# Kernel tuning notes

Hardware: AMD Instinct MI355X
Metric: run time of the kernel (lower is better)

The kernel has to match this reference:

```python
import jax, jax.numpy as jnp
import numpy as np

FIRE_RATE = 0.5
ANGLE = 0.0

def _sobel_kernels(angle=ANGLE):
    dx = np.outer([1, 2, 1], [-1, 0, 1]) / 8.0
    dy = dx.T
    c = np.cos(angle * np.pi / 180.0)
    s = np.sin(angle * np.pi / 180.0)
    w1 = (c * dx - s * dy).astype(np.float32)
    w2 = (s * dx + c * dy).astype(np.float32)
    # torch applies conv after transpose(1,3) so its spatial axes are (W,H);
    # transposing kernels makes our NHWC conv over (H,W) match exactly.
    return jnp.asarray(w1.T), jnp.asarray(w2.T)

def _depthwise3x3(x, w):
    # x: [B,H,W,C], w: [3,3] shared across all C channels (groups=C)
    C = x.shape[-1]
    k = jnp.tile(w[:, :, None, None], (1, 1, 1, C))  # [3,3,1,C] HWIO
    return jax.lax.conv_general_dilated(
        x, k, window_strides=(1, 1), padding='SAME',
        dimension_numbers=('NHWC', 'HWIO', 'NHWC'),
        feature_group_count=C)

def setup_inputs() -> dict:
    key = jax.random.key(0)
    k1, k2, k3 = jax.random.split(key, 3)
    B, H, W, C, HID = 8, 256, 256, 16, 128
    x = jax.random.uniform(k1, (B, H, W, C), dtype=jnp.float32)
    # xavier-uniform-like init for fc0/fc1
    lim0 = float(np.sqrt(6.0 / (3 * C + HID)))
    lim1 = float(np.sqrt(6.0 / (HID + C)))
    W0 = jax.random.uniform(k2, (HID, 3 * C), minval=-lim0, maxval=lim0, dtype=jnp.float32)
    b0 = jnp.zeros((HID,), dtype=jnp.float32)
    W1 = jax.random.uniform(k3, (C, HID), minval=-lim1, maxval=lim1, dtype=jnp.float32)
    return {'x': x, 'W0': W0, 'b0': b0, 'W1': W1, 'steps': 2}

def reference(x, W0, b0, W1, steps):
    w1, w2 = _sobel_kernels()
    key = jax.random.key(42)
    for step in range(steps):
        # perceive: identity + two depthwise sobel filters -> [B,H,W,3C]
        y = jnp.concatenate([x, _depthwise3x3(x, w1), _depthwise3x3(x, w2)], axis=-1)
        # per-cell MLP
        h = jax.nn.relu(jnp.einsum('bhwk,ok->bhwo', y, W0) + b0)
        dx = jnp.einsum('bhwo,co->bhwc', h, W1)
        # stochastic fire-rate mask [B,H,W,1]
        mk = jax.random.fold_in(key, step)
        mask = (jax.random.uniform(mk, dx.shape[:3] + (1,)) > FIRE_RATE).astype(dx.dtype)
        new = x + dx * mask
        # only channels 3: are updated (first 3 channels stay fixed)
        x = jnp.concatenate([x[..., :3], new[..., 3:]], axis=-1)
    return x
```

## Files before the change

### kernel.cpp

```cpp
#include <hip/hip_runtime.h>
#include <hip/hip_bf16.h>
#include <stdint.h>


#define NB 8
#define NH 256
#define NW 256
#define NC 16
#define WOFF 65536

typedef __attribute__((ext_vector_type(8))) short short8;
typedef __attribute__((ext_vector_type(4))) float floatx4;

__host__ __device__ inline void tf2x32(uint32_t k0, uint32_t k1,
                                       uint32_t x0, uint32_t x1,
                                       uint32_t& o0, uint32_t& o1) {
  const uint32_t ks2 = k0 ^ k1 ^ 0x1BD11BDAu;
  x0 += k0; x1 += k1;
#define RL(v, d) (((v) << (d)) | ((v) >> (32 - (d))))
#define R4(a, b, c, d)                          \
  x0 += x1; x1 = RL(x1, a); x1 ^= x0;           \
  x0 += x1; x1 = RL(x1, b); x1 ^= x0;           \
  x0 += x1; x1 = RL(x1, c); x1 ^= x0;           \
  x0 += x1; x1 = RL(x1, d); x1 ^= x0;
  R4(13, 15, 26, 6);  x0 += k1;  x1 += ks2 + 1u;
  R4(17, 29, 16, 24); x0 += ks2; x1 += k0 + 2u;
  R4(13, 15, 26, 6);  x0 += k0;  x1 += k1 + 3u;
  R4(17, 29, 16, 24); x0 += k1;  x1 += ks2 + 4u;
  R4(13, 15, 26, 6);  x0 += ks2; x1 += k0 + 5u;
#undef R4
#undef RL
  o0 = x0; o1 = x1;
}

__device__ inline short bfr(float x) {
  __hip_bfloat16 h = __float2bfloat16(x);
  return *reinterpret_cast<short*>(&h);
}

__global__ __launch_bounds__(64) void ca_prep(
    const float* __restrict__ W0, const float* __restrict__ b0,
    const float* __restrict__ W1, short* __restrict__ wbuf) {
  const int lane = threadIdx.x;
  const int c15 = lane & 15;
  const int g = lane >> 4;
  const int fi = blockIdx.x;
  short8 f;
  if (fi < 16) {
    const int n = fi >> 1;
    const int o = 16 * n + c15;
    if ((fi & 1) == 0) {
      const float s0 = (g < 2) ? 1.0f : 0.125f;
      const float* p = W0 + o * 48 + 8 * g;
      const floatx4 v0 = *reinterpret_cast<const floatx4*>(p);
      const floatx4 v1 = *reinterpret_cast<const floatx4*>(p + 4);
      f[0] = bfr(v0.x * s0); f[1] = bfr(v0.y * s0);
      f[2] = bfr(v0.z * s0); f[3] = bfr(v0.w * s0);
      f[4] = bfr(v1.x * s0); f[5] = bfr(v1.y * s0);
      f[6] = bfr(v1.z * s0); f[7] = bfr(v1.w * s0);
    } else {
      if (g < 2) {
        const float* p1 = W0 + o * 48 + 32 + 8 * g;
        const floatx4 u0 = *reinterpret_cast<const floatx4*>(p1);
        const floatx4 u1 = *reinterpret_cast<const floatx4*>(p1 + 4);
        f[0] = bfr(u0.x * 0.125f); f[1] = bfr(u0.y * 0.125f);
        f[2] = bfr(u0.z * 0.125f); f[3] = bfr(u0.w * 0.125f);
        f[4] = bfr(u1.x * 0.125f); f[5] = bfr(u1.y * 0.125f);
        f[6] = bfr(u1.z * 0.125f); f[7] = bfr(u1.w * 0.125f);
      } else {
#pragma unroll
        for (int j = 0; j < 8; ++j) f[j] = 0;
        if (g == 2) f[0] = bfr(b0[o]);
      }
    }
  } else {
    const int s = fi - 16;
    const float* p = W1 + c15 * 128;
#pragma unroll
    for (int j = 0; j < 8; ++j)
      f[j] = bfr(p[32 * s + 16 * (j >> 2) + 4 * g + (j & 3)]);
  }
  reinterpret_cast<short8*>(wbuf)[fi * 64 + lane] = f;
}

template <bool PRE>
__global__ __launch_bounds__(64, 2) void ca_step(
    const float* __restrict__ xin, float* __restrict__ xout,
    const float* __restrict__ W0, const float* __restrict__ b0,
    const float* __restrict__ W1, const short* __restrict__ wfrag,
    uint32_t fk0, uint32_t fk1) {
  __shared__ float xs[2][6 * 18 * 16];

  const int tid = threadIdx.x;
  const int bt = blockIdx.x;
  const int wt = bt & 15;
  const int ht16 = (bt >> 4) & 15;
  const int b = bt >> 8;
  const int h0 = ht16 * 16;
  const int w0 = wt * 16;

  const int lane = tid;
  const int c15 = lane & 15;
  const int g = lane >> 4;

  auto xsaddr = [&](float* base, int row, int col, int chunk) -> floatx4* {
    const int off = (row * 18 + col) * 64 + ((chunk ^ ((col >> 1) & 3)) << 4);
    return reinterpret_cast<floatx4*>(reinterpret_cast<char*>(base) + off);
  };

  short8 w0f[8][2];
  short8 w1f[4];
  if constexpr (PRE) {
    const short8* wf = reinterpret_cast<const short8*>(wfrag);
#pragma unroll
    for (int n = 0; n < 8; ++n) {
      w0f[n][0] = wf[(2 * n) * 64 + lane];
      w0f[n][1] = wf[(2 * n + 1) * 64 + lane];
    }
#pragma unroll
    for (int s = 0; s < 4; ++s) w1f[s] = wf[(16 + s) * 64 + lane];
  } else {
    const float s0 = (g < 2) ? 1.0f : 0.125f;
#pragma unroll
    for (int n = 0; n < 8; ++n) {
      const int o = 16 * n + c15;
      const float* p = W0 + o * 48 + 8 * g;
      const floatx4 v0 = *reinterpret_cast<const floatx4*>(p);
      const floatx4 v1 = *reinterpret_cast<const floatx4*>(p + 4);
      short8 f;
      f[0] = bfr(v0.x * s0); f[1] = bfr(v0.y * s0);
      f[2] = bfr(v0.z * s0); f[3] = bfr(v0.w * s0);
      f[4] = bfr(v1.x * s0); f[5] = bfr(v1.y * s0);
      f[6] = bfr(v1.z * s0); f[7] = bfr(v1.w * s0);
      w0f[n][0] = f;
      short8 f1;
      if (g < 2) {
        const float* p1 = W0 + o * 48 + 32 + 8 * g;
        const floatx4 u0 = *reinterpret_cast<const floatx4*>(p1);
        const floatx4 u1 = *reinterpret_cast<const floatx4*>(p1 + 4);
        f1[0] = bfr(u0.x * 0.125f); f1[1] = bfr(u0.y * 0.125f);
        f1[2] = bfr(u0.z * 0.125f); f1[3] = bfr(u0.w * 0.125f);
        f1[4] = bfr(u1.x * 0.125f); f1[5] = bfr(u1.y * 0.125f);
        f1[6] = bfr(u1.z * 0.125f); f1[7] = bfr(u1.w * 0.125f);
      } else {
#pragma unroll
        for (int j = 0; j < 8; ++j) f1[j] = 0;
        if (g == 2) f1[0] = bfr(b0[o]);
      }
      w0f[n][1] = f1;
    }
#pragma unroll
    for (int s = 0; s < 4; ++s) {
      const float* p = W1 + c15 * 128;
      short8 f;
#pragma unroll
      for (int j = 0; j < 8; ++j)
        f[j] = bfr(p[32 * s + 16 * (j >> 2) + 4 * g + (j & 3)]);
      w1f[s] = f;
    }
  }

  const int cc = 2 * (g & 1);
  const bool lo = (g < 2);
  const int col = 1 + c15;

  auto load_ph = [&](int h0t, floatx4* stg) {
#pragma unroll
    for (int i = 0; i < 7; ++i) {
      const int f = lane + 64 * i;
      floatx4 v = {0.f, 0.f, 0.f, 0.f};
      if (f < 432) {
        const int row = f / 72;
        const int rem = f - row * 72;
        const int cl = rem >> 2;
        const int q = rem & 3;
        const int gh = h0t - 1 + row;
        const int gw = w0 - 1 + cl;
        if ((unsigned)gh < (unsigned)NH && (unsigned)gw < (unsigned)NW)
          v = *reinterpret_cast<const floatx4*>(
              xin + (((size_t)b * NH + gh) * NW + gw) * NC + 4 * q);
      }
      stg[i] = v;
    }
  };
  auto write_ph = [&](float* buf, const floatx4* stg) {
#pragma unroll
    for (int i = 0; i < 7; ++i) {
      const int f = lane + 64 * i;
      if (f < 432) {
        const int row = f / 72;
        const int rem = f - row * 72;
        const int cl = rem >> 2;
        const int q = rem & 3;
        *xsaddr(buf, row, cl, q) = stg[i];
      }
    }
  };

#define PART(DST, ROW)                                                       \
  {                                                                          \
    const floatx4 L0 = *xsaddr(xsb, (ROW), col - 1, cc);                     \
    const floatx4 L1 = *xsaddr(xsb, (ROW), col - 1, cc + 1);                 \
    const floatx4 C0 = *xsaddr(xsb, (ROW), col, cc);                         \
    const floatx4 C1 = *xsaddr(xsb, (ROW), col, cc + 1);                     \
    const floatx4 R0 = *xsaddr(xsb, (ROW), col + 1, cc);                     \
    const floatx4 R1 = *xsaddr(xsb, (ROW), col + 1, cc + 1);                 \
    DST[0] = lo ? (R0.x - L0.x) : (L0.x + 2.f * C0.x + R0.x);                \
    DST[1] = lo ? (R0.y - L0.y) : (L0.y + 2.f * C0.y + R0.y);                \
    DST[2] = lo ? (R0.z - L0.z) : (L0.z + 2.f * C0.z + R0.z);                \
    DST[3] = lo ? (R0.w - L0.w) : (L0.w + 2.f * C0.w + R0.w);                \
    DST[4] = lo ? (R1.x - L1.x) : (L1.x + 2.f * C1.x + R1.x);                \
    DST[5] = lo ? (R1.y - L1.y) : (L1.y + 2.f * C1.y + R1.y);                \
    DST[6] = lo ? (R1.z - L1.z) : (L1.z + 2.f * C1.z + R1.z);                \
    DST[7] = lo ? (R1.w - L1.w) : (L1.w + 2.f * C1.w + R1.w);                \
  }

#define MTSTEP(MTI, HP, HC, HN)                                              \
  {                                                                          \
    const int r = 1 + (MTI);                                                 \
    const floatx4 xc0 = *xsaddr(xsb, r, col, cc);                            \
    const floatx4 xc1 = *xsaddr(xsb, r, col, cc + 1);                        \
    const float xcv[8] = {xc0.x, xc0.y, xc0.z, xc0.w,                        \
                          xc1.x, xc1.y, xc1.z, xc1.w};                       \
    short8 a0, a1;                                                           \
    _Pragma("unroll")                                                        \
    for (int j = 0; j < 8; ++j) {                                            \
      const float comb =                                                     \
          lo ? (HP[j] + 2.f * HC[j] + HN[j]) : (HN[j] - HP[j]);              \
      const short sb = bfr(comb);                                            \
      a0[j] = lo ? bfr(xcv[j]) : sb;                                         \
      a1[j] = lo ? sb : (short)0;                                            \
    }                                                                        \
    if (g == 2) a1[0] = bfr(1.0f);                                           \
    floatx4 acc[8];                                                          \
    _Pragma("unroll")                                                        \
    for (int n = 0; n < 8; ++n) acc[n] = floatx4{0.f, 0.f, 0.f, 0.f};        \
    _Pragma("unroll")                                                        \
    for (int n = 0; n < 8; ++n)                                              \
      acc[n] = __builtin_amdgcn_mfma_f32_16x16x32_bf16(w0f[n][0], a0,        \
                                                       acc[n], 0, 0, 0);     \
    _Pragma("unroll")                                                        \
    for (int n = 0; n < 8; ++n)                                              \
      acc[n] = __builtin_amdgcn_mfma_f32_16x16x32_bf16(w0f[n][1], a1,        \
                                                       acc[n], 0, 0, 0);     \
    floatx4 acc2 = {0.f, 0.f, 0.f, 0.f};                                     \
    _Pragma("unroll")                                                        \
    for (int s = 0; s < 4; ++s) {                                            \
      short8 b2;                                                             \
      _Pragma("unroll")                                                      \
      for (int j = 0; j < 8; ++j)                                            \
        b2[j] = bfr(fmaxf(acc[2 * s + (j >> 2)][j & 3], 0.f));               \
      acc2 = __builtin_amdgcn_mfma_f32_16x16x32_bf16(w1f[s], b2,             \
                                                     acc2, 0, 0, 0);         \
    }                                                                        \
    const floatx4 xv = *xsaddr(xsb, r, col, g);                              \
    const float mk = (float)((mball >> (16 * (MTI) + c15)) & 1ull);          \
    const float mk03 = (g == 0) ? 0.f : mk;                                  \
    floatx4 ov;                                                              \
    ov.x = xv.x + acc2.x * mk03;                                             \
    ov.y = xv.y + acc2.y * mk03;                                             \
    ov.z = xv.z + acc2.z * mk03;                                             \
    ov.w = xv.w + acc2.w * mk;                                               \
    const size_t cellg = ((size_t)(b * NH + h0t + (MTI))) * NW + w0 + c15;   \
    *reinterpret_cast<floatx4*>(xout + cellg * NC + 4 * g) = ov;             \
  }

  {
    floatx4 s0[7];
    load_ph(h0, s0);
    write_ph(reinterpret_cast<float*>(xs[0]), s0);
  }
  __syncthreads();

  int cur = 0;
#pragma unroll 1
  for (int t = 0; t < 4; ++t) {
    const int h0t = h0 + 4 * t;

    floatx4 stg[7];
    if (t < 3) {
      load_ph(h0t + 4, stg);
      asm volatile("" ::: "memory");
    }

    uint64_t mball;
    {
      const int cellg = (b * NH + h0t + (lane >> 4)) * NW + w0 + c15;
      uint32_t r0, r1;
      tf2x32(fk0, fk1, 0u, (uint32_t)cellg, r0, r1);
      const uint32_t bits = r0 ^ r1;
      const float u = __uint_as_float((bits >> 9) | 0x3F800000u) - 1.0f;
      mball = __ballot(u > 0.5f);
    }

    float* xsb = reinterpret_cast<float*>(xs[cur]);

    float hpA[8], hpB[8], hpC[8];
    PART(hpA, 0)
    PART(hpB, 1)
    PART(hpC, 2)
    MTSTEP(0, hpA, hpB, hpC)
    PART(hpA, 3)
    MTSTEP(1, hpB, hpC, hpA)
    PART(hpB, 4)
    MTSTEP(2, hpC, hpA, hpB)
    PART(hpC, 5)
    MTSTEP(3, hpA, hpB, hpC)

    if (t < 3) {
      __syncthreads();
      write_ph(reinterpret_cast<float*>(xs[cur ^ 1]), stg);
      __syncthreads();
      cur ^= 1;
    }
  }
#undef PART
#undef MTSTEP
}

extern "C" void kernel_launch(void* const* d_in, const int* in_sizes, int n_in,
                              void* d_out, int out_size, void* d_ws, size_t ws_size,
                              hipStream_t stream) {
  const float* x  = (const float*)d_in[0];
  const float* W0 = (const float*)d_in[1];
  const float* b0 = (const float*)d_in[2];
  const float* W1 = (const float*)d_in[3];
  float* out = (float*)d_out;

  const size_t tmp_bytes = (size_t)NB * NH * NW * NC * 4;
  const bool pre = ws_size >= (size_t)WOFF + tmp_bytes;
  short* wbuf = (short*)d_ws;
  float* tmp = pre ? (float*)((char*)d_ws + WOFF) : (float*)d_ws;

  uint32_t fa0, fa1, fb0, fb1;
  tf2x32(0u, 42u, 0u, 0u, fa0, fa1);
  tf2x32(0u, 42u, 0u, 1u, fb0, fb1);

  dim3 grid(NB * (NH / 16) * (NW / 16)), block(64);
  if (pre) {
    ca_prep<<<20, 64, 0, stream>>>(W0, b0, W1, wbuf);
    ca_step<true><<<grid, block, 0, stream>>>(x, tmp, W0, b0, W1, wbuf, fa0, fa1);
    ca_step<true><<<grid, block, 0, stream>>>(tmp, out, W0, b0, W1, wbuf, fb0, fb1);
  } else {
    ca_step<false><<<grid, block, 0, stream>>>(x, tmp, W0, b0, W1, nullptr, fa0, fa1);
    ca_step<false><<<grid, block, 0, stream>>>(tmp, out, W0, b0, W1, nullptr, fb0, fb1);
  }
}
```

Measured before the change: 57.79 us.

## Load full 18x18 halo tile once and fully unroll row sweep

Replaces the double-buffered 6-row phase pipeline with a single load of the whole 18x18x16 tile into LDS, followed by one barrier and a fully unrolled 16-row rolling stencil/MFMA sweep. Center values are now carried in registers from the stencil pass instead of being re-read from LDS. This removes the per-phase barriers and the duplicated halo-row loads. In exchange it drops the overlap of global loads with compute and raises LDS use per block from about 13.8 KB to about 20.7 KB, which could reduce occupancy.

Measured after the change: 90.16 us. 56.0% more time.

```diff
diff --git a/kernel.cpp b/kernel.cpp
--- a/kernel.cpp
+++ b/kernel.cpp
@@ -89,7 +89,7 @@
     const float* __restrict__ W0, const float* __restrict__ b0,
     const float* __restrict__ W1, const short* __restrict__ wfrag,
     uint32_t fk0, uint32_t fk1) {
-  __shared__ float xs[2][6 * 18 * 16];
+  __shared__ float xs[18 * 18 * 16];
 
   const int tid = threadIdx.x;
   const int bt = blockIdx.x;
@@ -103,9 +103,9 @@
   const int c15 = lane & 15;
   const int g = lane >> 4;
 
-  auto xsaddr = [&](float* base, int row, int col, int chunk) -> floatx4* {
+  auto xsaddr = [&](int row, int col, int chunk) -> floatx4* {
     const int off = (row * 18 + col) * 64 + ((chunk ^ ((col >> 1) & 3)) << 4);
-    return reinterpret_cast<floatx4*>(reinterpret_cast<char*>(base) + off);
+    return reinterpret_cast<floatx4*>(reinterpret_cast<char*>(xs) + off);
   };
 
   short8 w0f[8][2];
@@ -164,47 +164,31 @@
   const bool lo = (g < 2);
   const int col = 1 + c15;
 
-  auto load_ph = [&](int h0t, floatx4* stg) {
-#pragma unroll
-    for (int i = 0; i < 7; ++i) {
-      const int f = lane + 64 * i;
-      floatx4 v = {0.f, 0.f, 0.f, 0.f};
-      if (f < 432) {
-        const int row = f / 72;
-        const int rem = f - row * 72;
-        const int cl = rem >> 2;
-        const int q = rem & 3;
-        const int gh = h0t - 1 + row;
-        const int gw = w0 - 1 + cl;
-        if ((unsigned)gh < (unsigned)NH && (unsigned)gw < (unsigned)NW)
-          v = *reinterpret_cast<const floatx4*>(
-              xin + (((size_t)b * NH + gh) * NW + gw) * NC + 4 * q);
-      }
-      stg[i] = v;
-    }
-  };
-  auto write_ph = [&](float* buf, const floatx4* stg) {
-#pragma unroll
-    for (int i = 0; i < 7; ++i) {
-      const int f = lane + 64 * i;
-      if (f < 432) {
-        const int row = f / 72;
-        const int rem = f - row * 72;
-        const int cl = rem >> 2;
-        const int q = rem & 3;
-        *xsaddr(buf, row, cl, q) = stg[i];
-      }
-    }
-  };
-
-#define PART(DST, ROW)                                                       \
+  for (int f = lane; f < 18 * 18 * 4; f += 64) {
+    const int row = f / 72;
+    const int rem = f - row * 72;
+    const int cl = rem >> 2;
+    const int q = rem & 3;
+    const int gh = h0 - 1 + row;
+    const int gw = w0 - 1 + cl;
+    floatx4 v = {0.f, 0.f, 0.f, 0.f};
+    if ((unsigned)gh < (unsigned)NH && (unsigned)gw < (unsigned)NW)
+      v = *reinterpret_cast<const floatx4*>(
+          xin + (((size_t)b * NH + gh) * NW + gw) * NC + 4 * q);
+    *xsaddr(row, cl, q) = v;
+  }
+  __syncthreads();
+
+  uint64_t mball;
+
+#define PART(DST, CEN, ROW)                                                  \
   {                                                                          \
-    const floatx4 L0 = *xsaddr(xsb, (ROW), col - 1, cc);                     \
-    const floatx4 L1 = *xsaddr(xsb, (ROW), col - 1, cc + 1);                 \
-    const floatx4 C0 = *xsaddr(xsb, (ROW), col, cc);                         \
-    const floatx4 C1 = *xsaddr(xsb, (ROW), col, cc + 1);                     \
-    const floatx4 R0 = *xsaddr(xsb, (ROW), col + 1, cc);                     \
-    const floatx4 R1 = *xsaddr(xsb, (ROW), col + 1, cc + 1);                 \
+    const floatx4 L0 = *xsaddr((ROW), col - 1, cc);                          \
+    const floatx4 L1 = *xsaddr((ROW), col - 1, cc + 1);                      \
+    const floatx4 C0 = *xsaddr((ROW), col, cc);                              \
+    const floatx4 C1 = *xsaddr((ROW), col, cc + 1);                          \
+    const floatx4 R0 = *xsaddr((ROW), col + 1, cc);                          \
+    const floatx4 R1 = *xsaddr((ROW), col + 1, cc + 1);                      \
     DST[0] = lo ? (R0.x - L0.x) : (L0.x + 2.f * C0.x + R0.x);                \
     DST[1] = lo ? (R0.y - L0.y) : (L0.y + 2.f * C0.y + R0.y);                \
     DST[2] = lo ? (R0.z - L0.z) : (L0.z + 2.f * C0.z + R0.z);                \
@@ -213,22 +197,19 @@
     DST[5] = lo ? (R1.y - L1.y) : (L1.y + 2.f * C1.y + R1.y);                \
     DST[6] = lo ? (R1.z - L1.z) : (L1.z + 2.f * C1.z + R1.z);                \
     DST[7] = lo ? (R1.w - L1.w) : (L1.w + 2.f * C1.w + R1.w);                \
-  }
-
-#define MTSTEP(MTI, HP, HC, HN)                                              \
+    CEN[0] = C0.x; CEN[1] = C0.y; CEN[2] = C0.z; CEN[3] = C0.w;              \
+    CEN[4] = C1.x; CEN[5] = C1.y; CEN[6] = C1.z; CEN[7] = C1.w;              \
+  }
+
+#define MTSTEP(K, HP, HC, HN, CN)                                            \
   {                                                                          \
-    const int r = 1 + (MTI);                                                 \
-    const floatx4 xc0 = *xsaddr(xsb, r, col, cc);                            \
-    const floatx4 xc1 = *xsaddr(xsb, r, col, cc + 1);                        \
-    const float xcv[8] = {xc0.x, xc0.y, xc0.z, xc0.w,                        \
-                          xc1.x, xc1.y, xc1.z, xc1.w};                       \
     short8 a0, a1;                                                           \
     _Pragma("unroll")                                                        \
     for (int j = 0; j < 8; ++j) {                                            \
       const float comb =                                                     \
           lo ? (HP[j] + 2.f * HC[j] + HN[j]) : (HN[j] - HP[j]);              \
       const short sb = bfr(comb);                                            \
-      a0[j] = lo ? bfr(xcv[j]) : sb;                                         \
+      a0[j] = lo ? bfr(CN[j]) : sb;                                          \
       a1[j] = lo ? sb : (short)0;                                            \
     }                                                                        \
     if (g == 2) a1[0] = bfr(1.0f);                                           \
@@ -253,69 +234,54 @@
       acc2 = __builtin_amdgcn_mfma_f32_16x16x32_bf16(w1f[s], b2,             \
                                                      acc2, 0, 0, 0);         \
     }                                                                        \
-    const floatx4 xv = *xsaddr(xsb, r, col, g);                              \
-    const float mk = (float)((mball >> (16 * (MTI) + c15)) & 1ull);          \
+    const floatx4 xv = *xsaddr((K) + 1, col, g);                             \
+    const float mk = (float)((mball >> (16 * ((K) & 3) + c15)) & 1ull);      \
     const float mk03 = (g == 0) ? 0.f : mk;                                  \
     floatx4 ov;                                                              \
     ov.x = xv.x + acc2.x * mk03;                                             \
     ov.y = xv.y + acc2.y * mk03;                                             \
     ov.z = xv.z + acc2.z * mk03;                                             \
     ov.w = xv.w + acc2.w * mk;                                               \
-    const size_t cellg = ((size_t)(b * NH + h0t + (MTI))) * NW + w0 + c15;   \
+    const size_t cellg = ((size_t)(b * NH + h0 + (K))) * NW + w0 + c15;      \
     *reinterpret_cast<floatx4*>(xout + cellg * NC + 4 * g) = ov;             \
   }
 
-  {
-    floatx4 s0[7];
-    load_ph(h0, s0);
-    write_ph(reinterpret_cast<float*>(xs[0]), s0);
-  }
-  __syncthreads();
-
-  int cur = 0;
-#pragma unroll 1
-  for (int t = 0; t < 4; ++t) {
-    const int h0t = h0 + 4 * t;
-
-    floatx4 stg[7];
-    if (t < 3) {
-      load_ph(h0t + 4, stg);
-      asm volatile("" ::: "memory");
-    }
-
-    uint64_t mball;
-    {
-      const int cellg = (b * NH + h0t + (lane >> 4)) * NW + w0 + c15;
-      uint32_t r0, r1;
-      tf2x32(fk0, fk1, 0u, (uint32_t)cellg, r0, r1);
-      const uint32_t bits = r0 ^ r1;
-      const float u = __uint_as_float((bits >> 9) | 0x3F800000u) - 1.0f;
-      mball = __ballot(u > 0.5f);
-    }
-
-    float* xsb = reinterpret_cast<float*>(xs[cur]);
-
-    float hpA[8], hpB[8], hpC[8];
-    PART(hpA, 0)
-    PART(hpB, 1)
-    PART(hpC, 2)
-    MTSTEP(0, hpA, hpB, hpC)
-    PART(hpA, 3)
-    MTSTEP(1, hpB, hpC, hpA)
-    PART(hpB, 4)
-    MTSTEP(2, hpC, hpA, hpB)
-    PART(hpC, 5)
-    MTSTEP(3, hpA, hpB, hpC)
-
-    if (t < 3) {
-      __syncthreads();
-      write_ph(reinterpret_cast<float*>(xs[cur ^ 1]), stg);
-      __syncthreads();
-      cur ^= 1;
-    }
-  }
+#define MBALL(T)                                                             \
+  {                                                                          \
+    const int cellg = (b * NH + h0 + 4 * (T) + (lane >> 4)) * NW + w0 + c15; \
+    uint32_t r0, r1;                                                         \
+    tf2x32(fk0, fk1, 0u, (uint32_t)cellg, r0, r1);                           \
+    const uint32_t bits = r0 ^ r1;                                           \
+    const float u = __uint_as_float((bits >> 9) | 0x3F800000u) - 1.0f;       \
+    mball = __ballot(u > 0.5f);                                              \
+  }
+
+  float hpA[8], hpB[8], hpC[8], cnA[8], cnB[8], cnC[8];
+  PART(hpA, cnA, 0) PART(hpB, cnB, 1) PART(hpC, cnC, 2)
+  MBALL(0)
+  MTSTEP(0, hpA, hpB, hpC, cnB)  PART(hpA, cnA, 3)
+  MTSTEP(1, hpB, hpC, hpA, cnC)  PART(hpB, cnB, 4)
+  MTSTEP(2, hpC, hpA, hpB, cnA)  PART(hpC, cnC, 5)
+  MTSTEP(3, hpA, hpB, hpC, cnB)  PART(hpA, cnA, 6)
+  MBALL(1)
+  MTSTEP(4, hpB, hpC, hpA, cnC)  PART(hpB, cnB, 7)
+  MTSTEP(5, hpC, hpA, hpB, cnA)  PART(hpC, cnC, 8)
+  MTSTEP(6, hpA, hpB, hpC, cnB)  PART(hpA, cnA, 9)
+  MTSTEP(7, hpB, hpC, hpA, cnC)  PART(hpB, cnB, 10)
+  MBALL(2)
+  MTSTEP(8, hpC, hpA, hpB, cnA)  PART(hpC, cnC, 11)
+  MTSTEP(9, hpA, hpB, hpC, cnB)  PART(hpA, cnA, 12)
+  MTSTEP(10, hpB, hpC, hpA, cnC) PART(hpB, cnB, 13)
+  MTSTEP(11, hpC, hpA, hpB, cnA) PART(hpC, cnC, 14)
+  MBALL(3)
+  MTSTEP(12, hpA, hpB, hpC, cnB) PART(hpA, cnA, 15)
+  MTSTEP(13, hpB, hpC, hpA, cnC) PART(hpB, cnB, 16)
+  MTSTEP(14, hpC, hpA, hpB, cnA) PART(hpC, cnC, 17)
+  MTSTEP(15, hpA, hpB, hpC, cnB)
+
 #undef PART
 #undef MTSTEP
+#undef MBALL
 }
 
 extern "C" void kernel_launch(void* const* d_in, const int* in_sizes, int n_in,
```
